# Kernel optimization log

Hardware: AMD Instinct MI355X
Metric: run time of the kernel (lower is better)

## Reference

```python
import jax, jax.numpy as jnp
import numpy as np

N = 8192
D_MODEL = 256
D_K = 128
NUM_MOL = 512  # molecule_index values in [0, NUM_MOL); output rows = max(idx)+1, fixed here for jit


def setup_inputs() -> dict:
    key = jax.random.key(0)
    k1, k2, k3, k4, k5, k6, k7, k8 = jax.random.split(key, 8)
    fragments = jax.random.normal(k1, (N, D_MODEL), dtype=jnp.float32)
    molecule_index = jnp.sort(jax.random.randint(k2, (N,), 0, NUM_MOL, dtype=jnp.int64))
    s = 1.0 / np.sqrt(D_MODEL)
    Wq = jax.random.uniform(k3, (D_MODEL, D_K), jnp.float32, -s, s)
    bq = jax.random.uniform(k4, (D_K,), jnp.float32, -s, s)
    Wk = jax.random.uniform(k5, (D_MODEL, D_K), jnp.float32, -s, s)
    bk = jax.random.uniform(k6, (D_K,), jnp.float32, -s, s)
    Wv = jax.random.uniform(k7, (D_MODEL, D_K), jnp.float32, -s, s)
    bv = jax.random.uniform(k8, (D_K,), jnp.float32, -s, s)
    return {"fragments": fragments, "molecule_index": molecule_index,
            "Wq": Wq, "bq": bq, "Wk": Wk, "bk": bk, "Wv": Wv, "bv": bv}


def reference(fragments, molecule_index, Wq, bq, Wk, bk, Wv, bv):
    scale = jnp.asarray(np.sqrt(D_K), fragments.dtype)
    Q = fragments @ Wq + bq  # [N, d_k]
    K = fragments @ Wk + bk
    V = fragments @ Wv + bv
    scores = (Q / scale) @ K.T  # [N, N]
    same_mol = molecule_index[:, None] == molecule_index[None, :]
    scores = jnp.where(same_mol, scores, -jnp.inf)
    weights = jax.nn.softmax(scores, axis=-1)  # block-diagonal rows
    out = weights @ V  # [N, d_k]
    # scatter_add per-molecule pooling
    mol_emb = jax.ops.segment_sum(out, molecule_index, num_segments=NUM_MOL)
    return mol_emb
```

## Files before the change

### kernel.cpp

```cpp
#include <hip/hip_runtime.h>
#include <hip/hip_bf16.h>

#define D_MODEL 256
#define D_K 128
#define CH 48
#define NEG_BF16 ((unsigned short)0xFF7F)

typedef short bf16x8 __attribute__((ext_vector_type(8)));
typedef float f32x4 __attribute__((ext_vector_type(4)));

__device__ inline unsigned short f2bf(float x) {
    union { float f; unsigned u; } v; v.f = x;
    unsigned r = v.u + 0x7FFFu + ((v.u >> 16) & 1u);
    return (unsigned short)(r >> 16);
}
__device__ inline float bf2f(unsigned short h) {
    union { unsigned u; float f; } v; v.u = ((unsigned)h) << 16; return v.f;
}

#define AT_BYTE(r, c2) (((r) << 9) + ((((c2) << 1)) ^ (((r) & 7) << 4)))
#define QB_OFF 32768
#define KB_OFF 50176
#define S_OFF  67584
#define RINV_OFF 76288
#define CSUM_OFF 76544
#define EMB_OFF  76800

__device__ __forceinline__ int wave_lb(const int* __restrict__ p, int stride, int n, int val, int guess) {
    const int lane = threadIdx.x & 63;
    int base = guess - 32;
    while (true) {
        int idx = base + lane;
        int v;
        if (idx < 0)        v = -2147483647 - 1;
        else if (idx >= n)  v = 2147483647;
        else                v = p[(size_t)idx * stride];
        unsigned long long ge = __ballot(v >= val);
        if (ge == 0ULL) { base += 64; continue; }
        int v0 = __shfl(v, 0);
        if (v0 >= val && base > 0) { base -= 63; continue; }
        return base + (__ffsll((unsigned long long)ge) - 1);
    }
}

__device__ __forceinline__ bf16x8 w_frag(const float* __restrict__ W, int cc, int k0, int g) {
    const float* p = W + (size_t)(k0 + g * 8) * D_K + cc;
    unsigned short t8[8];
    #pragma unroll
    for (int j = 0; j < 8; ++j) t8[j] = f2bf(p[(size_t)j * D_K]);
    return *(const bf16x8*)t8;
}

template<int NRT>
__device__ __forceinline__ void qkv_tiles(
    const unsigned char* lds,
    const float* __restrict__ Wq, const float* __restrict__ Wk, const float* __restrict__ Wv,
    int wave, int lr, int g, f32x4 (&acc)[3][NRT])
{
    #pragma unroll
    for (int cl = 0; cl < 3; ++cl) {
        const int ct = wave + cl * 8;
        const int which = ct >> 3, cc = (ct & 7) * 16 + lr;
        const float* W = which == 0 ? Wq : (which == 1 ? Wk : Wv);
        #pragma unroll
        for (int k0 = 0; k0 < 8; ++k0) {
            bf16x8 bf = w_frag(W, cc, k0 * 32, g);
            #pragma unroll
            for (int rt = 0; rt < NRT; ++rt) {
                bf16x8 af = *(const bf16x8*)(lds + AT_BYTE(rt * 16 + lr, k0 * 32 + g * 8));
                acc[cl][rt] = __builtin_amdgcn_mfma_f32_16x16x32_bf16(af, bf, acc[cl][rt], 0, 0, 0);
            }
        }
    }
}

template<int NRT>
__device__ __forceinline__ void fast_pair(
    const float* __restrict__ A,
    const float* __restrict__ Wq, const float* __restrict__ bq,
    const float* __restrict__ Wk, const float* __restrict__ bk,
    const float* __restrict__ Wv, const float* __restrict__ bv,
    float* __restrict__ out, unsigned char* lds,
    int s, int mtot, int c1, int mol0, int mol1, bool w0, bool w1)
{
    unsigned short* Qb = (unsigned short*)(lds + QB_OFF);
    unsigned short* Kb = (unsigned short*)(lds + KB_OFF);
    unsigned short* Vb = (unsigned short*)(lds);
    unsigned short* S  = (unsigned short*)(lds + S_OFF);
    float* rinv = (float*)(lds + RINV_OFF);
    float* csum = (float*)(lds + CSUM_OFF);
    float* emb  = (float*)(lds + EMB_OFF);

    const int tid = threadIdx.x;
    const int wave = tid >> 6, lane = tid & 63;
    const int lr = lane & 15, g = lane >> 4;

    #pragma unroll
    for (int it = 0; it < NRT * 2; ++it) {
        int eidx = tid * 4 + it * 2048;
        int r = eidx >> 8, c = eidx & 255;
        float4 a;
        if (r < mtot) a = *(const float4*)&A[(size_t)(s + r) * D_MODEL + c];
        else          a = make_float4(0.f, 0.f, 0.f, 0.f);
        unsigned short o[4] = {f2bf(a.x), f2bf(a.y), f2bf(a.z), f2bf(a.w)};
        *(unsigned long long*)(lds + AT_BYTE(r, c)) = *(const unsigned long long*)o;
    }
    __syncthreads();

    f32x4 acc[3][NRT];
    #pragma unroll
    for (int i = 0; i < 3; ++i)
        #pragma unroll
        for (int j = 0; j < NRT; ++j) acc[i][j] = {0.f, 0.f, 0.f, 0.f};
    qkv_tiles<NRT>(lds, Wq, Wk, Wv, wave, lr, g, acc);
    __syncthreads();

    const float qs = 0.08838834764831845f;
    #pragma unroll
    for (int cl = 0; cl < 3; ++cl) {
        int ct = wave + cl * 8;
        int which = ct >> 3;
        int col = (ct & 7) * 16 + lr;
        const float* bsrc = which == 0 ? bq : (which == 1 ? bk : bv);
        float bb = bsrc[col];
        float sc = which == 0 ? qs : 1.f;
        unsigned short* dst = which == 0 ? Qb : (which == 1 ? Kb : Vb);
        #pragma unroll
        for (int rt = 0; rt < NRT; ++rt) {
            int rbase = rt * 16 + g * 4;
            #pragma unroll
            for (int r = 0; r < 4; ++r)
                dst[(rbase + r) * 136 + col] = f2bf((acc[cl][rt][r] + bb) * sc);
        }
    }
    __syncthreads();

    for (int job = wave; job < NRT * NRT; job += 8) {
        int ti = job / NRT, tj = job % NRT;
        f32x4 sa = {0.f, 0.f, 0.f, 0.f};
        #pragma unroll
        for (int kk = 0; kk < 4; ++kk) {
            bf16x8 qf = *(const bf16x8*)&Qb[(ti * 16 + lr) * 136 + kk * 32 + g * 8];
            bf16x8 kf = *(const bf16x8*)&Kb[(tj * 16 + lr) * 136 + kk * 32 + g * 8];
            sa = __builtin_amdgcn_mfma_f32_16x16x32_bf16(qf, kf, sa, 0, 0, 0);
        }
        int jcol = tj * 16 + lr, ibase = ti * 16 + g * 4;
        bool jside = jcol < c1;
        #pragma unroll
        for (int r = 0; r < 4; ++r) {
            bool same = ((ibase + r) < c1) == jside;
            S[(ibase + r) * 68 + jcol] = same ? f2bf(sa[r]) : NEG_BF16;
        }
    }
    __syncthreads();

    {
        int row = tid >> 2, sub = tid & 3;
        if (row < mtot) {
            float mx = -3.4e38f;
            for (int j = sub; j < mtot; j += 4) mx = fmaxf(mx, bf2f(S[row * 68 + j]));
            mx = fmaxf(mx, __shfl_xor(mx, 1));
            mx = fmaxf(mx, __shfl_xor(mx, 2));
            float sum = 0.f;
            for (int j = sub; j < mtot; j += 4) {
                float ev = __expf(bf2f(S[row * 68 + j]) - mx);
                S[row * 68 + j] = f2bf(ev);
                sum += ev;
            }
            sum += __shfl_xor(sum, 1);
            sum += __shfl_xor(sum, 2);
            if (sub == 0) rinv[row] = 1.f / sum;
        }
    }
    __syncthreads();

    {
        int col = tid >> 2, sub = tid & 3;
        if (col < mtot) {
            float a = 0.f;
            for (int i = sub; i < mtot; i += 4) a += bf2f(S[i * 68 + col]) * rinv[i];
            a += __shfl_xor(a, 1);
            a += __shfl_xor(a, 2);
            if (sub == 0) csum[col] = a;
        }
    }
    __syncthreads();

    {
        int d = tid & 127, h = tid >> 7;
        float a = 0.f;
        for (int j = h; j < c1; j += 4) a += csum[j] * bf2f(Vb[j * 136 + d]);
        emb[h * D_K + d] = a;
        __syncthreads();
        if (w0 && tid < D_K)
            out[(size_t)mol0 * D_K + tid] = emb[tid] + emb[D_K + tid] + emb[2 * D_K + tid] + emb[3 * D_K + tid];
        __syncthreads();
        a = 0.f;
        for (int j = c1 + h; j < mtot; j += 4) a += csum[j] * bf2f(Vb[j * 136 + d]);
        emb[h * D_K + d] = a;
        __syncthreads();
        if (w1 && tid < D_K)
            out[(size_t)mol1 * D_K + tid] = emb[tid] + emb[D_K + tid] + emb[2 * D_K + tid] + emb[3 * D_K + tid];
    }
}

__device__ __forceinline__ void run_single(
    const float* __restrict__ A,
    const float* __restrict__ Wq, const float* __restrict__ bq,
    const float* __restrict__ Wk, const float* __restrict__ bk,
    const float* __restrict__ Wv, const float* __restrict__ bv,
    float* __restrict__ out, unsigned char* lds, int s, int m, int mol)
{
    if (m <= 16)      fast_pair<1>(A, Wq, bq, Wk, bk, Wv, bv, out, lds, s, m, m, mol, mol, true, false);
    else if (m <= 32) fast_pair<2>(A, Wq, bq, Wk, bk, Wv, bv, out, lds, s, m, m, mol, mol, true, false);
    else if (m <= 48) fast_pair<3>(A, Wq, bq, Wk, bk, Wv, bv, out, lds, s, m, m, mol, mol, true, false);
    else              fast_pair<4>(A, Wq, bq, Wk, bk, Wv, bv, out, lds, s, m, m, mol, mol, true, false);
}

__device__ void slow_stream(
    const float* __restrict__ A,
    const float* __restrict__ Wq, const float* __restrict__ bq,
    const float* __restrict__ Wk, const float* __restrict__ bk,
    const float* __restrict__ Wv, const float* __restrict__ bv,
    float* __restrict__ out, unsigned char* lds,
    float* __restrict__ Qw, float* __restrict__ Kw, float* __restrict__ Vw,
    float* __restrict__ ML, int s, int m, int mol, int n)
{
    const int tid = threadIdx.x;
    const int wave = tid >> 6, lane = tid & 63;
    const int lr = lane & 15, g = lane >> 4;
    const float qs = 0.08838834764831845f;
    float* emb = (float*)(lds + EMB_OFF);

    for (int r0 = 0; r0 < m; r0 += CH) {
        for (int it = 0; it < (CH * 256) / 2048; ++it) {
            int eidx = tid * 4 + it * 2048;
            int r = eidx >> 8, c = eidx & 255;
            float4 a;
            if (r0 + r < m) a = *(const float4*)&A[(size_t)(s + r0 + r) * D_MODEL + c];
            else            a = make_float4(0.f, 0.f, 0.f, 0.f);
            unsigned short o[4] = {f2bf(a.x), f2bf(a.y), f2bf(a.z), f2bf(a.w)};
            *(unsigned long long*)(lds + AT_BYTE(r, c)) = *(const unsigned long long*)o;
        }
        __syncthreads();

        f32x4 acc[3][3];
        #pragma unroll
        for (int i = 0; i < 3; ++i)
            #pragma unroll
            for (int j = 0; j < 3; ++j) acc[i][j] = {0.f, 0.f, 0.f, 0.f};
        qkv_tiles<3>(lds, Wq, Wk, Wv, wave, lr, g, acc);

        #pragma unroll
        for (int cl = 0; cl < 3; ++cl) {
            int ct = wave + cl * 8;
            int which = ct >> 3;
            int col = (ct & 7) * 16 + lr;
            const float* bsrc = which == 0 ? bq : (which == 1 ? bk : bv);
            float bb = bsrc[col];
            float sc = which == 0 ? qs : 1.f;
            float* dst = which == 0 ? Qw : (which == 1 ? Kw : Vw);
            #pragma unroll
            for (int rt = 0; rt < 3; ++rt) {
                int rbase = rt * 16 + g * 4;
                #pragma unroll
                for (int r = 0; r < 4; ++r) {
                    int lrow = rbase + r;
                    if (r0 + lrow < m)
                        dst[(size_t)(s + r0 + lrow) * D_K + col] = (acc[cl][rt][r] + bb) * sc;
                }
            }
        }
        __syncthreads();
    }

    if (tid < D_K) emb[tid] = 0.f;
    float* Mv = ML;
    float* Lv = ML + n;
    __threadfence();
    __syncthreads();

    for (int i = tid; i < m; i += 512) {
        const float4* q = (const float4*)(Qw + (size_t)(s + i) * D_K);
        float mx = -3.4e38f, sum = 0.f;
        for (int j = 0; j < m; ++j) {
            const float4* k = (const float4*)(Kw + (size_t)(s + j) * D_K);
            float sc = 0.f;
            #pragma unroll
            for (int t = 0; t < D_K / 4; ++t) {
                float4 a = q[t], b = k[t];
                sc += a.x * b.x + a.y * b.y + a.z * b.z + a.w * b.w;
            }
            if (sc > mx) { sum = sum * __expf(mx - sc) + 1.f; mx = sc; }
            else         { sum += __expf(sc - mx); }
        }
        Mv[s + i] = mx;
        Lv[s + i] = 1.f / sum;
    }
    __threadfence();
    __syncthreads();

    for (int j = tid; j < m; j += 512) {
        const float4* k = (const float4*)(Kw + (size_t)(s + j) * D_K);
        float cj = 0.f;
        for (int i = 0; i < m; ++i) {
            const float4* q = (const float4*)(Qw + (size_t)(s + i) * D_K);
            float sc = 0.f;
            #pragma unroll
            for (int t = 0; t < D_K / 4; ++t) {
                float4 a = q[t], b = k[t];
                sc += a.x * b.x + a.y * b.y + a.z * b.z + a.w * b.w;
            }
            cj += __expf(sc - Mv[s + i]) * Lv[s + i];
        }
        const float* v = Vw + (size_t)(s + j) * D_K;
        for (int d = 0; d < D_K; ++d) atomicAdd(&emb[d], cj * v[d]);
    }
    __syncthreads();
    if (tid < D_K) out[(size_t)mol * D_K + tid] = emb[tid];
}

__global__ __launch_bounds__(512, 1) void fused_pair(
    const float* __restrict__ A,
    const float* __restrict__ Wq, const float* __restrict__ bq,
    const float* __restrict__ Wk, const float* __restrict__ bk,
    const float* __restrict__ Wv, const float* __restrict__ bv,
    const int* __restrict__ midx,
    float* __restrict__ out,
    float* __restrict__ Qw, float* __restrict__ Kw, float* __restrict__ Vw,
    float* __restrict__ ML, int n, int nmol)
{
    __shared__ __align__(16) unsigned char lds[78848];
    int* se = (int*)(lds + RINV_OFF);

    const int tid = threadIdx.x;
    const int wave = tid >> 6;
    const int mol0 = blockIdx.x * 2;
    const int mol1 = mol0 + 1;
    const bool haveM1 = mol1 < nmol;

    const int stride = (midx[n - 1] == 0) ? 2 : 1;

    if (wave < 3) {
        int val = mol0 + wave;
        if (val > nmol) val = nmol;
        int r = wave_lb(midx, stride, n, val, (int)(((long long)val * n) / nmol));
        if ((tid & 63) == 0) se[wave] = r;
    }
    __syncthreads();
    const int s0 = se[0], s1 = se[1], e = se[2];
    __syncthreads();

    const int m0 = s1 - s0, m1 = e - s1, mtot = e - s0;
    const int c1 = m0;

    if (mtot == 0) {
        if (tid < D_K) out[(size_t)mol0 * D_K + tid] = 0.f;
        else if (haveM1 && tid < 2 * D_K) out[(size_t)mol1 * D_K + (tid - D_K)] = 0.f;
        return;
    }

    if (mtot <= 64) {
        if (mtot <= 16)      fast_pair<1>(A, Wq, bq, Wk, bk, Wv, bv, out, lds, s0, mtot, c1, mol0, mol1, true, haveM1);
        else if (mtot <= 32) fast_pair<2>(A, Wq, bq, Wk, bk, Wv, bv, out, lds, s0, mtot, c1, mol0, mol1, true, haveM1);
        else if (mtot <= 48) fast_pair<3>(A, Wq, bq, Wk, bk, Wv, bv, out, lds, s0, mtot, c1, mol0, mol1, true, haveM1);
        else                 fast_pair<4>(A, Wq, bq, Wk, bk, Wv, bv, out, lds, s0, mtot, c1, mol0, mol1, true, haveM1);
        return;
    }

    if (m0 <= 64) run_single(A, Wq, bq, Wk, bk, Wv, bv, out, lds, s0, m0, mol0);
    else          slow_stream(A, Wq, bq, Wk, bk, Wv, bv, out, lds, Qw, Kw, Vw, ML, s0, m0, mol0, n);
    __syncthreads();
    if (haveM1) {
        if (m1 == 0) { if (tid < D_K) out[(size_t)mol1 * D_K + tid] = 0.f; return; }
        if (m1 <= 64) run_single(A, Wq, bq, Wk, bk, Wv, bv, out, lds, s1, m1, mol1);
        else          slow_stream(A, Wq, bq, Wk, bk, Wv, bv, out, lds, Qw, Kw, Vw, ML, s1, m1, mol1, n);
    }
}

extern "C" void kernel_launch(void* const* d_in, const int* in_sizes, int n_in,
                              void* d_out, int out_size, void* d_ws, size_t ws_size,
                              hipStream_t stream) {
    const float* frag = (const float*)d_in[0];
    const int*   midx = (const int*)d_in[1];
    const float* Wq = (const float*)d_in[2];
    const float* bq = (const float*)d_in[3];
    const float* Wk = (const float*)d_in[4];
    const float* bk = (const float*)d_in[5];
    const float* Wv = (const float*)d_in[6];
    const float* bv = (const float*)d_in[7];
    float* out = (float*)d_out;

    const int n = in_sizes[1];
    const int nmol = out_size / D_K;

    float* Qw = (float*)d_ws;
    float* Kw = Qw + (size_t)n * D_K;
    float* Vw = Kw + (size_t)n * D_K;
    float* ML = Vw + (size_t)n * D_K;

    const int nblocks = (nmol + 1) / 2;
    fused_pair<<<nblocks, 512, 0, stream>>>(frag, Wq, bq, Wk, bk, Wv, bv, midx,
                                            out, Qw, Kw, Vw, ML, n, nmol);
}
```

Before: 17.20 us.

## Prefetch weight fragments before barrier and fuse Q/K/V MFMA per column tile

Each wave now owns one 16-column slice of Q, K and V at once. It loads and converts all 24 weight fragments into registers before the first barrier, overlapping that global-load latency with staging the fragment rows into LDS. V gets its own LDS region so it no longer aliases the A buffer, which lets the barrier after the QKV MFMAs go. The two per-molecule pooling passes are merged into one pass with separate partial sums. The changes raise register pressure and LDS size (98 KB), and the launch bounds now ask for 2 blocks per CU, which may cause spills or not fit.

```diff
diff --git a/kernel.cpp b/kernel.cpp
--- a/kernel.cpp
+++ b/kernel.cpp
@@ -21,10 +21,11 @@
 #define AT_BYTE(r, c2) (((r) << 9) + ((((c2) << 1)) ^ (((r) & 7) << 4)))
 #define QB_OFF 32768
 #define KB_OFF 50176
-#define S_OFF  67584
-#define RINV_OFF 76288
-#define CSUM_OFF 76544
-#define EMB_OFF  76800
+#define VB_OFF 67584
+#define S_OFF  84992
+#define RINV_OFF 93696
+#define CSUM_OFF 93952
+#define EMB_OFF  94208
 
 __device__ __forceinline__ int wave_lb(const int* __restrict__ p, int stride, int n, int val, int guess) {
     const int lane = threadIdx.x & 63;
@@ -52,29 +53,6 @@
 }
 
 template<int NRT>
-__device__ __forceinline__ void qkv_tiles(
-    const unsigned char* lds,
-    const float* __restrict__ Wq, const float* __restrict__ Wk, const float* __restrict__ Wv,
-    int wave, int lr, int g, f32x4 (&acc)[3][NRT])
-{
-    #pragma unroll
-    for (int cl = 0; cl < 3; ++cl) {
-        const int ct = wave + cl * 8;
-        const int which = ct >> 3, cc = (ct & 7) * 16 + lr;
-        const float* W = which == 0 ? Wq : (which == 1 ? Wk : Wv);
-        #pragma unroll
-        for (int k0 = 0; k0 < 8; ++k0) {
-            bf16x8 bf = w_frag(W, cc, k0 * 32, g);
-            #pragma unroll
-            for (int rt = 0; rt < NRT; ++rt) {
-                bf16x8 af = *(const bf16x8*)(lds + AT_BYTE(rt * 16 + lr, k0 * 32 + g * 8));
-                acc[cl][rt] = __builtin_amdgcn_mfma_f32_16x16x32_bf16(af, bf, acc[cl][rt], 0, 0, 0);
-            }
-        }
-    }
-}
-
-template<int NRT>
 __device__ __forceinline__ void fast_pair(
     const float* __restrict__ A,
     const float* __restrict__ Wq, const float* __restrict__ bq,
@@ -85,7 +63,7 @@
 {
     unsigned short* Qb = (unsigned short*)(lds + QB_OFF);
     unsigned short* Kb = (unsigned short*)(lds + KB_OFF);
-    unsigned short* Vb = (unsigned short*)(lds);
+    unsigned short* Vb = (unsigned short*)(lds + VB_OFF);
     unsigned short* S  = (unsigned short*)(lds + S_OFF);
     float* rinv = (float*)(lds + RINV_OFF);
     float* csum = (float*)(lds + CSUM_OFF);
@@ -94,6 +72,7 @@
     const int tid = threadIdx.x;
     const int wave = tid >> 6, lane = tid & 63;
     const int lr = lane & 15, g = lane >> 4;
+    const int cc = wave * 16 + lr;
 
     #pragma unroll
     for (int it = 0; it < NRT * 2; ++it) {
@@ -105,32 +84,42 @@
         unsigned short o[4] = {f2bf(a.x), f2bf(a.y), f2bf(a.z), f2bf(a.w)};
         *(unsigned long long*)(lds + AT_BYTE(r, c)) = *(const unsigned long long*)o;
     }
-    __syncthreads();
-
-    f32x4 acc[3][NRT];
+
+    bf16x8 wfq[8], wfk[8], wfv[8];
     #pragma unroll
-    for (int i = 0; i < 3; ++i)
-        #pragma unroll
-        for (int j = 0; j < NRT; ++j) acc[i][j] = {0.f, 0.f, 0.f, 0.f};
-    qkv_tiles<NRT>(lds, Wq, Wk, Wv, wave, lr, g, acc);
-    __syncthreads();
+    for (int k0 = 0; k0 < 8; ++k0) {
+        wfq[k0] = w_frag(Wq, cc, k0 * 32, g);
+        wfk[k0] = w_frag(Wk, cc, k0 * 32, g);
+        wfv[k0] = w_frag(Wv, cc, k0 * 32, g);
+    }
+    __syncthreads();
+
+    f32x4 accq[NRT], acck[NRT], accv[NRT];
+    #pragma unroll
+    for (int j = 0; j < NRT; ++j) { accq[j] = {0.f,0.f,0.f,0.f}; acck[j] = {0.f,0.f,0.f,0.f}; accv[j] = {0.f,0.f,0.f,0.f}; }
+    #pragma unroll
+    for (int k0 = 0; k0 < 8; ++k0) {
+        #pragma unroll
+        for (int rt = 0; rt < NRT; ++rt) {
+            bf16x8 af = *(const bf16x8*)(lds + AT_BYTE(rt * 16 + lr, k0 * 32 + g * 8));
+            accq[rt] = __builtin_amdgcn_mfma_f32_16x16x32_bf16(af, wfq[k0], accq[rt], 0, 0, 0);
+            acck[rt] = __builtin_amdgcn_mfma_f32_16x16x32_bf16(af, wfk[k0], acck[rt], 0, 0, 0);
+            accv[rt] = __builtin_amdgcn_mfma_f32_16x16x32_bf16(af, wfv[k0], accv[rt], 0, 0, 0);
+        }
+    }
 
     const float qs = 0.08838834764831845f;
-    #pragma unroll
-    for (int cl = 0; cl < 3; ++cl) {
-        int ct = wave + cl * 8;
-        int which = ct >> 3;
-        int col = (ct & 7) * 16 + lr;
-        const float* bsrc = which == 0 ? bq : (which == 1 ? bk : bv);
-        float bb = bsrc[col];
-        float sc = which == 0 ? qs : 1.f;
-        unsigned short* dst = which == 0 ? Qb : (which == 1 ? Kb : Vb);
+    {
+        float bbq = bq[cc] , bbk = bk[cc], bbv = bv[cc];
         #pragma unroll
         for (int rt = 0; rt < NRT; ++rt) {
             int rbase = rt * 16 + g * 4;
             #pragma unroll
-            for (int r = 0; r < 4; ++r)
-                dst[(rbase + r) * 136 + col] = f2bf((acc[cl][rt][r] + bb) * sc);
+            for (int r = 0; r < 4; ++r) {
+                Qb[(rbase + r) * 136 + cc] = f2bf((accq[rt][r] + bbq) * qs);
+                Kb[(rbase + r) * 136 + cc] = f2bf(acck[rt][r] + bbk);
+                Vb[(rbase + r) * 136 + cc] = f2bf(accv[rt][r] + bbv);
+            }
         }
     }
     __syncthreads();
@@ -187,20 +176,23 @@
     __syncthreads();
 
     {
-        int d = tid & 127, h = tid >> 7;
-        float a = 0.f;
-        for (int j = h; j < c1; j += 4) a += csum[j] * bf2f(Vb[j * 136 + d]);
-        emb[h * D_K + d] = a;
+        int d = tid & 127, h = (tid >> 7) & 3;
+        float a0 = 0.f, a1 = 0.f;
+        for (int j = h; j < mtot; j += 4) {
+            float t = csum[j] * bf2f(Vb[j * 136 + d]);
+            if (j < c1) a0 += t; else a1 += t;
+        }
+        emb[h * D_K + d] = a0;
+        emb[(4 + h) * D_K + d] = a1;
         __syncthreads();
-        if (w0 && tid < D_K)
-            out[(size_t)mol0 * D_K + tid] = emb[tid] + emb[D_K + tid] + emb[2 * D_K + tid] + emb[3 * D_K + tid];
-        __syncthreads();
-        a = 0.f;
-        for (int j = c1 + h; j < mtot; j += 4) a += csum[j] * bf2f(Vb[j * 136 + d]);
-        emb[h * D_K + d] = a;
-        __syncthreads();
-        if (w1 && tid < D_K)
-            out[(size_t)mol1 * D_K + tid] = emb[tid] + emb[D_K + tid] + emb[2 * D_K + tid] + emb[3 * D_K + tid];
+        if (tid < D_K) {
+            if (w0) out[(size_t)mol0 * D_K + tid] =
+                emb[tid] + emb[D_K + tid] + emb[2 * D_K + tid] + emb[3 * D_K + tid];
+        } else if (tid < 2 * D_K) {
+            int d1 = tid - D_K;
+            if (w1) out[(size_t)mol1 * D_K + d1] =
+                emb[4 * D_K + d1] + emb[5 * D_K + d1] + emb[6 * D_K + d1] + emb[7 * D_K + d1];
+        }
     }
 }
 
@@ -229,6 +221,7 @@
     const int tid = threadIdx.x;
     const int wave = tid >> 6, lane = tid & 63;
     const int lr = lane & 15, g = lane >> 4;
+    const int cc = wave * 16 + lr;
     const float qs = 0.08838834764831845f;
     float* emb = (float*)(lds + EMB_OFF);
 
@@ -244,30 +237,34 @@
         }
         __syncthreads();
 
-        f32x4 acc[3][3];
-        #pragma unroll
-        for (int i = 0; i < 3; ++i)
-            #pragma unroll
-            for (int j = 0; j < 3; ++j) acc[i][j] = {0.f, 0.f, 0.f, 0.f};
-        qkv_tiles<3>(lds, Wq, Wk, Wv, wave, lr, g, acc);
-
-        #pragma unroll
-        for (int cl = 0; cl < 3; ++cl) {
-            int ct = wave + cl * 8;
-            int which = ct >> 3;
-            int col = (ct & 7) * 16 + lr;
-            const float* bsrc = which == 0 ? bq : (which == 1 ? bk : bv);
-            float bb = bsrc[col];
-            float sc = which == 0 ? qs : 1.f;
-            float* dst = which == 0 ? Qw : (which == 1 ? Kw : Vw);
+        f32x4 accq[3], acck[3], accv[3];
+        #pragma unroll
+        for (int j = 0; j < 3; ++j) { accq[j] = {0.f,0.f,0.f,0.f}; acck[j] = {0.f,0.f,0.f,0.f}; accv[j] = {0.f,0.f,0.f,0.f}; }
+        #pragma unroll
+        for (int k0 = 0; k0 < 8; ++k0) {
+            bf16x8 fq = w_frag(Wq, cc, k0 * 32, g);
+            bf16x8 fk = w_frag(Wk, cc, k0 * 32, g);
+            bf16x8 fv = w_frag(Wv, cc, k0 * 32, g);
             #pragma unroll
             for (int rt = 0; rt < 3; ++rt) {
-                int rbase = rt * 16 + g * 4;
-                #pragma unroll
-                for (int r = 0; r < 4; ++r) {
-                    int lrow = rbase + r;
-                    if (r0 + lrow < m)
-                        dst[(size_t)(s + r0 + lrow) * D_K + col] = (acc[cl][rt][r] + bb) * sc;
+                bf16x8 af = *(const bf16x8*)(lds + AT_BYTE(rt * 16 + lr, k0 * 32 + g * 8));
+                accq[rt] = __builtin_amdgcn_mfma_f32_16x16x32_bf16(af, fq, accq[rt], 0, 0, 0);
+                acck[rt] = __builtin_amdgcn_mfma_f32_16x16x32_bf16(af, fk, acck[rt], 0, 0, 0);
+                accv[rt] = __builtin_amdgcn_mfma_f32_16x16x32_bf16(af, fv, accv[rt], 0, 0, 0);
+            }
+        }
+
+        float bbq = bq[cc], bbk = bk[cc], bbv = bv[cc];
+        #pragma unroll
+        for (int rt = 0; rt < 3; ++rt) {
+            int rbase = rt * 16 + g * 4;
+            #pragma unroll
+            for (int r = 0; r < 4; ++r) {
+                int lrow = rbase + r;
+                if (r0 + lrow < m) {
+                    Qw[(size_t)(s + r0 + lrow) * D_K + cc] = (accq[rt][r] + bbq) * qs;
+                    Kw[(size_t)(s + r0 + lrow) * D_K + cc] = acck[rt][r] + bbk;
+                    Vw[(size_t)(s + r0 + lrow) * D_K + cc] = accv[rt][r] + bbv;
                 }
             }
         }
@@ -320,7 +317,7 @@
     if (tid < D_K) out[(size_t)mol * D_K + tid] = emb[tid];
 }
 
-__global__ __launch_bounds__(512, 1) void fused_pair(
+__global__ __launch_bounds__(512, 2) void fused_pair(
     const float* __restrict__ A,
     const float* __restrict__ Wq, const float* __restrict__ bq,
     const float* __restrict__ Wk, const float* __restrict__ bk,
@@ -330,7 +327,7 @@
     float* __restrict__ Qw, float* __restrict__ Kw, float* __restrict__ Vw,
     float* __restrict__ ML, int n, int nmol)
 {
-    __shared__ __align__(16) unsigned char lds[78848];
+    __shared__ __align__(16) unsigned char lds[98304];
     int* se = (int*)(lds + RINV_OFF);
 
     const int tid = threadIdx.x;
@@ -349,8 +346,6 @@
     }
     __syncthreads();
     const int s0 = se[0], s1 = se[1], e = se[2];
-    __syncthreads();
-
     const int m0 = s1 - s0, m1 = e - s1, mtot = e - s0;
     const int c1 = m0;
 
```

Result: slower. 17.85 us (+3.8%).
